# Optimization experiments

Hardware: AMD Instinct MI355X
Metric: run time of the kernel (lower is better)

## Reference

```python
import jax, jax.numpy as jnp
import numpy as np

N_HEADS = 32
WINDOW = 128  # each query t attends keys max(0, t-window) .. t inclusive (window+1 keys)


def _sliding_window_attention(x, Wq, Wk, Wv, Wo, n_heads=N_HEADS, window=WINDOW):
    B, T, D = x.shape
    H, dk = n_heads, D // n_heads
    bs = window            # block size = window -> each query block sees exactly 2 key blocks
    assert T % bs == 0
    nb = T // bs

    def heads(y):  # [B,T,D] -> [B,H,T,dk]
        return y.reshape(B, T, H, dk).transpose(0, 2, 1, 3)

    q = heads(x @ Wq.T)
    k = heads(x @ Wk.T)
    v = heads(x @ Wv.T)

    # Block queries: [B,H,nb,bs,dk]
    qb = q.reshape(B, H, nb, bs, dk)
    # Pad one zero block in front of keys/values, then build per-block 2-block windows.
    zpad = jnp.zeros((B, H, bs, dk), dtype=x.dtype)
    kp = jnp.concatenate([zpad, k], axis=2).reshape(B, H, nb + 1, bs, dk)
    vp = jnp.concatenate([zpad, v], axis=2).reshape(B, H, nb + 1, bs, dk)
    kw = jnp.concatenate([kp[:, :, :-1], kp[:, :, 1:]], axis=3)  # [B,H,nb,2bs,dk]
    vw = jnp.concatenate([vp[:, :, :-1], vp[:, :, 1:]], axis=3)

    scale = 1.0 / np.sqrt(dk).astype(np.float32)
    # scores: [B,H,nb,bs,2bs]
    scores = jnp.einsum('bhnrd,bhncd->bhnrc', qb, kw) * scale

    # Banded causal mask. Query global pos = i*bs + r, key global pos = (i-1)*bs + c.
    i = jnp.arange(nb)[:, None, None]
    r = jnp.arange(bs)[None, :, None]
    c = jnp.arange(2 * bs)[None, None, :]
    dist = (bs + r) - c                       # qpos - keypos
    key_global = i * bs - bs + c
    valid = (dist >= 0) & (dist <= window) & (key_global >= 0)  # [nb,bs,2bs]

    scores = jnp.where(valid[None, None], scores, jnp.finfo(scores.dtype).min)
    probs = jax.nn.softmax(scores, axis=-1)
    out = jnp.einsum('bhnrc,bhncd->bhnrd', probs, vw)           # [B,H,nb,bs,dk]
    out = out.reshape(B, H, T, dk).transpose(0, 2, 1, 3).reshape(B, T, D)
    return out @ Wo.T


def setup_inputs() -> dict:
    key = jax.random.key(0)
    ks = jax.random.split(key, 5)
    B, T, D = 2, 4096, 2048
    w_std = 0.02
    return {
        'x':  jax.random.normal(ks[0], (B, T, D), dtype=jnp.float32),
        'Wq': jax.random.normal(ks[1], (D, D), dtype=jnp.float32) * w_std,
        'Wk': jax.random.normal(ks[2], (D, D), dtype=jnp.float32) * w_std,
        'Wv': jax.random.normal(ks[3], (D, D), dtype=jnp.float32) * w_std,
        'Wo': jax.random.normal(ks[4], (D, D), dtype=jnp.float32) * w_std,
    }


def reference(x, Wq, Wk, Wv, Wo):
    return _sliding_window_attention(x, Wq, Wk, Wv, Wo)
```

## Files before the change

kernel.cpp:

```cpp
#include <hip/hip_runtime.h>
#include <hip/hip_bf16.h>

typedef __attribute__((ext_vector_type(8))) short bf16x8;
typedef __attribute__((ext_vector_type(8))) unsigned short ushort8;
typedef __attribute__((ext_vector_type(4))) float f32x4;
typedef __attribute__((ext_vector_type(2))) unsigned int u32x2;

#define MFMA16(a, b, c) __builtin_amdgcn_mfma_f32_16x16x32_bf16(a, b, c, 0, 0, 0)
#define CFENCE() asm volatile("" ::: "memory")

__device__ __forceinline__ unsigned short f2bf(float x) {
    unsigned u = __builtin_bit_cast(unsigned, x);
    u += 0x7FFFu + ((u >> 16) & 1u);
    return (unsigned short)(u >> 16);
}

__device__ __forceinline__ float fexp2(float x) {
#if __has_builtin(__builtin_amdgcn_exp2f)
    return __builtin_amdgcn_exp2f(x);
#else
    return exp2f(x);
#endif
}

__device__ __forceinline__ void gload16(const void* g, void* l) {
    __builtin_amdgcn_global_load_lds((const __attribute__((address_space(1))) void*)g,
                                     (__attribute__((address_space(3))) void*)l, 16, 0, 0);
}

__device__ __forceinline__ void bar() {
    asm volatile("" ::: "memory");
    __builtin_amdgcn_s_barrier();
    asm volatile("" ::: "memory");
}

#define WAITL() do { asm volatile("s_waitcnt lgkmcnt(0)" ::: "memory"); \
                     __builtin_amdgcn_sched_barrier(0); } while (0)

__global__ void cvt_f32_bf16(const float* __restrict__ src, unsigned short* __restrict__ dst, int n8) {
    int stride = gridDim.x * blockDim.x;
    for (int i = blockIdx.x * blockDim.x + threadIdx.x; i < n8; i += stride) {
        const float4* s = reinterpret_cast<const float4*>(src) + (size_t)i * 2;
        float4 a = s[0], b = s[1];
        ushort8 o;
        o[0] = f2bf(a.x); o[1] = f2bf(a.y); o[2] = f2bf(a.z); o[3] = f2bf(a.w);
        o[4] = f2bf(b.x); o[5] = f2bf(b.y); o[6] = f2bf(b.z); o[7] = f2bf(b.w);
        *(reinterpret_cast<ushort8*>(dst) + i) = o;
    }
}

#define QUAD(mg, ng, bfv)                                                         \
    do {                                                                          \
        _Pragma("unroll") for (int mm = 0; mm < 4; ++mm)                          \
        _Pragma("unroll") for (int nn = 0; nn < 2; ++nn)                          \
        _Pragma("unroll") for (int kk = 0; kk < 2; ++kk)                          \
            acc[(mg) * 4 + mm][(ng) * 2 + nn] =                                   \
                MFMA16(af[mm][kk], bfv[nn][kk], acc[(mg) * 4 + mm][(ng) * 2 + nn]); \
    } while (0)

template <int MODE>
__global__ __launch_bounds__(512, 2)
void gemm256(const unsigned short* __restrict__ A, const unsigned short* __restrict__ B,
             void* __restrict__ C, int M, int N, int K) {
    __shared__ char sm[131072];

    const int tid  = threadIdx.x;
    const int wid  = tid >> 6, lane = tid & 63;
    const int wr   = wid >> 2, wc = wid & 3;
    const int lrow = lane >> 4, lcol = lane & 15;

    const int flat = blockIdx.x;
    const int s = (flat & 7) * (gridDim.x >> 3) + (flat >> 3);
    const int nbn = N >> 8;
    const int bm = s / nbn, bn = s % nbn;

    const int srow = wid * 8 + (lane >> 3);
    const int scol = ((lane & 7) ^ ((lane >> 3) & 7)) * 8;
    const unsigned short* aS = A + (size_t)(bm * 256 + srow) * K + scol;
    const unsigned short* bS = B + (size_t)(bn * 256 + srow) * K + scol;
    const int ldsW = wid * 1024;

    auto stageA = [&](int d, int h, int t) {
#pragma unroll
        for (int q = 0; q < 2; ++q)
            gload16(aS + (size_t)(h * 128 + q * 64) * K + t * 64,
                    sm + d * 32768 + h * 16384 + ldsW + q * 8192);
    };
    auto stageB = [&](int d, int h, int t) {
#pragma unroll
        for (int q = 0; q < 2; ++q)
            gload16(bS + (size_t)(h * 128 + q * 64) * K + t * 64,
                    sm + 65536 + d * 32768 + h * 16384 + ldsW + q * 8192);
    };

    const int swz0 = (lrow * 16) ^ ((lcol & 7) << 4);
    const int swz1 = (64 + lrow * 16) ^ ((lcol & 7) << 4);
    const int ra = wr * 16 + lcol;
    const int rb = wc * 16 + lcol;

    bf16x8 af[4][2], bl[2][2], bh[2][2];
    auto loadA = [&](int d, int mg) {
#pragma unroll
        for (int mm = 0; mm < 4; ++mm) {
            af[mm][0] = *(const bf16x8*)(sm + d * 32768 + mg * 16384 + (mm * 32 + ra) * 128 + swz0);
            af[mm][1] = *(const bf16x8*)(sm + d * 32768 + mg * 16384 + (mm * 32 + ra) * 128 + swz1);
        }
    };
    auto loadB = [&](int d, int ng, bf16x8 (&bfv)[2][2]) {
#pragma unroll
        for (int nn = 0; nn < 2; ++nn) {
            bfv[nn][0] = *(const bf16x8*)(sm + 65536 + d * 32768 + ng * 16384 + (nn * 64 + rb) * 128 + swz0);
            bfv[nn][1] = *(const bf16x8*)(sm + 65536 + d * 32768 + ng * 16384 + (nn * 64 + rb) * 128 + swz1);
        }
    };

    f32x4 acc[8][4] = {};

    stageA(0, 0, 0); stageB(0, 0, 0); stageB(0, 1, 0); stageA(0, 1, 0);
    stageA(1, 0, 1); stageB(1, 0, 1); stageB(1, 1, 1);
    asm volatile("s_waitcnt vmcnt(6)" ::: "memory");
    bar();

    const int NI = K / 128;
#pragma unroll 1
    for (int i = 0; i < NI; ++i) {
        const int t0 = 2 * i;
        const bool last = (i == NI - 1);
        loadA(0, 0); loadB(0, 0, bl);
        stageA(1, 1, t0 + 1);
        bar(); WAITL();
        __builtin_amdgcn_s_setprio(1); QUAD(0, 0, bl); __builtin_amdgcn_s_setprio(0);
        bar();
        loadB(0, 1, bh);
        if (!last) stageA(0, 0, t0 + 2);
        bar(); WAITL();
        __builtin_amdgcn_s_setprio(1); QUAD(0, 1, bh); __builtin_amdgcn_s_setprio(0);
        bar();
        loadA(0, 1);
        if (!last) stageB(0, 0, t0 + 2);
        bar(); WAITL();
        __builtin_amdgcn_s_setprio(1); QUAD(1, 0, bl); __builtin_amdgcn_s_setprio(0);
        bar();
        if (!last) stageB(0, 1, t0 + 2);
        bar();
        __builtin_amdgcn_s_setprio(1); QUAD(1, 1, bh); __builtin_amdgcn_s_setprio(0);
        if (last) asm volatile("s_waitcnt vmcnt(0)" ::: "memory");
        else      asm volatile("s_waitcnt vmcnt(6)" ::: "memory");
        bar();
        loadA(1, 0); loadB(1, 0, bl);
        if (!last) stageA(0, 1, t0 + 2);
        bar(); WAITL();
        __builtin_amdgcn_s_setprio(1); QUAD(0, 0, bl); __builtin_amdgcn_s_setprio(0);
        bar();
        loadB(1, 1, bh);
        if (!last) stageA(1, 0, t0 + 3);
        bar(); WAITL();
        __builtin_amdgcn_s_setprio(1); QUAD(0, 1, bh); __builtin_amdgcn_s_setprio(0);
        bar();
        loadA(1, 1);
        if (!last) stageB(1, 0, t0 + 3);
        bar(); WAITL();
        __builtin_amdgcn_s_setprio(1); QUAD(1, 0, bl); __builtin_amdgcn_s_setprio(0);
        bar();
        if (!last) stageB(1, 1, t0 + 3);
        bar();
        __builtin_amdgcn_s_setprio(1); QUAD(1, 1, bh); __builtin_amdgcn_s_setprio(0);
        if (!last) asm volatile("s_waitcnt vmcnt(6)" ::: "memory");
        bar();
    }

    const size_t row0 = (size_t)bm * 256 + wr * 16 + lrow * 4;
    if (MODE == 1) {
        const int col0 = bn * 256 + wc * 16 + lcol;
#pragma unroll
        for (int m = 0; m < 8; ++m)
#pragma unroll
            for (int n = 0; n < 4; ++n)
#pragma unroll
                for (int r = 0; r < 4; ++r)
                    ((float*)C)[(row0 + m * 32 + r) * N + col0 + n * 64] = acc[m][n][r];
    } else {
        const int seg = (bn * 256) >> 11;
        const int coll = bn * 256 - seg * 2048 + wc * 16 + lcol;
        unsigned short* out = (unsigned short*)C + (size_t)seg * 16777216ull;
#pragma unroll
        for (int m = 0; m < 8; ++m)
#pragma unroll
            for (int n = 0; n < 4; ++n)
#pragma unroll
                for (int r = 0; r < 4; ++r)
                    out[(row0 + m * 32 + r) * 2048 + coll + n * 64] = f2bf(acc[m][n][r]);
    }
}

__global__ __launch_bounds__(256, 3)
void swa_attn(const unsigned short* __restrict__ Qb, const unsigned short* __restrict__ Kb,
              const unsigned short* __restrict__ Vb, unsigned short* __restrict__ Ob) {
    constexpr int T = 4096, D = 2048;
    constexpr float SC = 0.18033688011112042f;

    __shared__ unsigned short vt[64][136];
    __shared__ unsigned short pls[4][32][40];

    const int bid  = blockIdx.x;
    const int flat = (bid & 7) * 256 + (bid >> 3);
    const int i = flat & 31, h = (flat >> 5) & 31, b = flat >> 10;

    const int tid = threadIdx.x, wid = tid >> 6, lane = tid & 63;
    const int lcol = lane & 15, lrow = lane >> 4;

    const unsigned short* qp = Qb + (size_t)b * T * D + h * 64;
    const unsigned short* kp = Kb + (size_t)b * T * D + h * 64;
    const unsigned short* vp = Vb + (size_t)b * T * D + h * 64;

    const int t0 = (i == 0) ? 1 : 0;

    const int q0 = i * 128 + wid * 32;
    bf16x8 aq[2][2];
#pragma unroll
    for (int qg = 0; qg < 2; ++qg)
#pragma unroll
        for (int kf = 0; kf < 2; ++kf)
            aq[qg][kf] = *(const bf16x8*)(qp + (size_t)(q0 + qg * 16 + lcol) * D + kf * 32 + lrow * 8);

    f32x4 oacc[2][4] = {};
    float mrun[2] = {-1e30f, -1e30f}, lrun[2] = {0.f, 0.f};

#pragma unroll 1
    for (int t = t0; t < 2; ++t) {
        const int kt0 = (i - 1 + t) * 128;

#pragma unroll
        for (int it = 0; it < 4; ++it) {
            int e = it * 2048 + tid * 8;
            int kr = e >> 6;
            int dc = e & 63;
            bf16x8 v = *(const bf16x8*)(vp + (size_t)(kt0 + kr) * D + dc);
#pragma unroll
            for (int j = 0; j < 8; ++j) vt[dc + j][kr] = (unsigned short)v[j];
        }

        f32x4 s[2][8];
#pragma unroll
        for (int n = 0; n < 8; ++n) {
            const unsigned short* krow = kp + (size_t)(kt0 + n * 16 + lcol) * D + lrow * 8;
            bf16x8 k0 = *(const bf16x8*)(krow);
            bf16x8 k1 = *(const bf16x8*)(krow + 32);
            f32x4 z = {0.f, 0.f, 0.f, 0.f};
            s[0][n] = MFMA16(k1, aq[0][1], MFMA16(k0, aq[0][0], z));
            s[1][n] = MFMA16(k1, aq[1][1], MFMA16(k0, aq[1][0], z));
        }

#pragma unroll
        for (int qg = 0; qg < 2; ++qg) {
            const int q = wid * 32 + qg * 16 + lcol;
#pragma unroll
            for (int n = 0; n < 8; ++n) {
                const int cb = t * 128 + n * 16 + lrow * 4 - q;
#pragma unroll
                for (int r = 0; r < 4; ++r)
                    s[qg][n][r] = ((unsigned)(cb + r) <= 128u) ? s[qg][n][r] * SC : -1e30f;
            }
        }

#pragma unroll
        for (int qg = 0; qg < 2; ++qg) {
            float cm = -1e30f;
#pragma unroll
            for (int n = 0; n < 8; ++n)
#pragma unroll
                for (int r = 0; r < 4; ++r) cm = fmaxf(cm, s[qg][n][r]);
            cm = fmaxf(cm, __shfl_xor(cm, 16));
            cm = fmaxf(cm, __shfl_xor(cm, 32));
            const float mn = fmaxf(mrun[qg], cm);
            const float sf = fexp2(mrun[qg] - mn);
            mrun[qg] = mn;
            float rs = 0.f;
#pragma unroll
            for (int n = 0; n < 8; ++n)
#pragma unroll
                for (int r = 0; r < 4; ++r) {
                    float p = fexp2(s[qg][n][r] - mn);
                    s[qg][n][r] = p;
                    rs += p;
                }
            rs += __shfl_xor(rs, 16);
            rs += __shfl_xor(rs, 32);
            lrun[qg] = lrun[qg] * sf + rs;
#pragma unroll
            for (int nf = 0; nf < 4; ++nf) oacc[qg][nf] *= sf;
        }

        __syncthreads();

#pragma unroll
        for (int ks = 0; ks < 4; ++ks) {
            CFENCE();
#pragma unroll
            for (int qg = 0; qg < 2; ++qg) {
                unsigned short* prow = &pls[wid][qg * 16 + lcol][0];
#pragma unroll
                for (int r = 0; r < 4; ++r) {
                    prow[4 * lrow + r]      = f2bf(s[qg][2 * ks][r]);
                    prow[16 + 4 * lrow + r] = f2bf(s[qg][2 * ks + 1][r]);
                }
            }
            CFENCE();
            WAITL();
            bf16x8 pf0 = *(const bf16x8*)&pls[wid][lcol][lrow * 8];
            bf16x8 pf1 = *(const bf16x8*)&pls[wid][16 + lcol][lrow * 8];
#pragma unroll
            for (int nf = 0; nf < 4; ++nf) {
                bf16x8 av = *(const bf16x8*)&vt[nf * 16 + lcol][ks * 32 + lrow * 8];
                oacc[0][nf] = MFMA16(av, pf0, oacc[0][nf]);
                oacc[1][nf] = MFMA16(av, pf1, oacc[1][nf]);
            }
            CFENCE();
        }

        __syncthreads();
    }

#pragma unroll
    for (int qg = 0; qg < 2; ++qg) {
        const float inv = 1.f / lrun[qg];
        const int tok = i * 128 + wid * 32 + qg * 16 + lcol;
        unsigned short* orow = Ob + (size_t)(b * T + tok) * D + h * 64;
#pragma unroll
        for (int nf = 0; nf < 4; ++nf) {
            unsigned o0 = (unsigned)f2bf(oacc[qg][nf][0] * inv) |
                          ((unsigned)f2bf(oacc[qg][nf][1] * inv) << 16);
            unsigned o1 = (unsigned)f2bf(oacc[qg][nf][2] * inv) |
                          ((unsigned)f2bf(oacc[qg][nf][3] * inv) << 16);
            *(u32x2*)(orow + nf * 16 + lrow * 4) = (u32x2){o0, o1};
        }
    }
}

extern "C" void kernel_launch(void* const* d_in, const int* in_sizes, int n_in,
                              void* d_out, int out_size, void* d_ws, size_t ws_size,
                              hipStream_t stream) {
    const float* x  = (const float*)d_in[0];
    const float* Wq = (const float*)d_in[1];
    const float* Wk = (const float*)d_in[2];
    const float* Wv = (const float*)d_in[3];
    const float* Wo = (const float*)d_in[4];

    constexpr int B = 2, T = 4096, D = 2048;
    constexpr int M = B * T;
    constexpr size_t XE = (size_t)M * D;
    constexpr size_t WE = (size_t)D * D;

    char* ws = (char*)d_ws;
    unsigned short* xb  = (unsigned short*)(ws);
    unsigned short* wqb = (unsigned short*)(ws + XE * 2);
    unsigned short* wkb = (unsigned short*)(ws + XE * 2 + WE * 2);
    unsigned short* wvb = (unsigned short*)(ws + XE * 2 + WE * 4);
    unsigned short* wob = (unsigned short*)(ws + XE * 2 + WE * 6);
    unsigned short* qb  = (unsigned short*)(ws + XE * 2 + WE * 8);
    unsigned short* kb  = (unsigned short*)(ws + XE * 4 + WE * 8);
    unsigned short* vb  = (unsigned short*)(ws + XE * 6 + WE * 8);
    unsigned short* ab  = (unsigned short*)(ws + XE * 8 + WE * 8);

    cvt_f32_bf16<<<2048, 256, 0, stream>>>(x,  xb,  (int)(XE / 8));
    cvt_f32_bf16<<<2048, 256, 0, stream>>>(Wq, wqb, (int)(WE / 8));
    cvt_f32_bf16<<<2048, 256, 0, stream>>>(Wk, wkb, (int)(WE / 8));
    cvt_f32_bf16<<<2048, 256, 0, stream>>>(Wv, wvb, (int)(WE / 8));
    cvt_f32_bf16<<<2048, 256, 0, stream>>>(Wo, wob, (int)(WE / 8));

    gemm256<2><<<dim3((M / 256) * (6144 / 256)), 512, 0, stream>>>(xb, wqb, qb, M, 6144, D);

    swa_attn<<<dim3(2048), 256, 0, stream>>>(qb, kb, vb, ab);

    gemm256<1><<<dim3((M / 256) * (D / 256)), 512, 0, stream>>>(ab, wob, d_out, M, D, D);
}
```

Measured before the change: 358.3 us.

## Merge conversion launches, remap GEMM tiles per XCD, restage A prefetch

Replaces five separate fp32-to-bf16 conversion launches with one kernel covering x and all four weights in a contiguous workspace, which removes launch overhead and tail effects. Changes the GEMM block-to-tile mapping so each XCD owns a contiguous band of M rows and walks across N. This aims to improve L2 reuse of A tiles within an XCD. Moves the A-half prefetch (stageA(1,1)/(0,1)) into the same stage slot as the B prefetch and raises the vmcnt wait from 6 to 8, changing how global loads overlap with MFMA work.

```diff
diff --git a/kernel.cpp b/kernel.cpp
--- a/kernel.cpp
+++ b/kernel.cpp
@@ -37,10 +37,25 @@
 #define WAITL() do { asm volatile("s_waitcnt lgkmcnt(0)" ::: "memory"); \
                      __builtin_amdgcn_sched_barrier(0); } while (0)
 
-__global__ void cvt_f32_bf16(const float* __restrict__ src, unsigned short* __restrict__ dst, int n8) {
+__global__ void cvt_all(const float* __restrict__ x, const float* __restrict__ wq,
+                        const float* __restrict__ wk, const float* __restrict__ wv,
+                        const float* __restrict__ wo, unsigned short* __restrict__ dst,
+                        int total8) {
+    constexpr int XE8 = 2097152;
+    constexpr int WE8 = 524288;
     int stride = gridDim.x * blockDim.x;
-    for (int i = blockIdx.x * blockDim.x + threadIdx.x; i < n8; i += stride) {
-        const float4* s = reinterpret_cast<const float4*>(src) + (size_t)i * 2;
+    for (int i = blockIdx.x * blockDim.x + threadIdx.x; i < total8; i += stride) {
+        const float* src;
+        if (i < XE8) {
+            src = x + (size_t)i * 8;
+        } else {
+            int k = i - XE8;
+            int seg = k >> 19;
+            int off = k & (WE8 - 1);
+            const float* w = (seg == 0) ? wq : (seg == 1) ? wk : (seg == 2) ? wv : wo;
+            src = w + (size_t)off * 8;
+        }
+        const float4* s = (const float4*)src;
         float4 a = s[0], b = s[1];
         ushort8 o;
         o[0] = f2bf(a.x); o[1] = f2bf(a.y); o[2] = f2bf(a.z); o[3] = f2bf(a.w);
@@ -69,10 +84,12 @@
     const int wr   = wid >> 2, wc = wid & 3;
     const int lrow = lane >> 4, lcol = lane & 15;
 
-    const int flat = blockIdx.x;
-    const int s = (flat & 7) * (gridDim.x >> 3) + (flat >> 3);
-    const int nbn = N >> 8;
-    const int bm = s / nbn, bn = s % nbn;
+    const int nbm = M >> 8;
+    const int rpx = nbm >> 3;
+    const int xcd = blockIdx.x & 7;
+    const int l   = blockIdx.x >> 3;
+    const int bm  = xcd * rpx + (l & (rpx - 1));
+    const int bn  = l / rpx;
 
     const int srow = wid * 8 + (lane >> 3);
     const int scol = ((lane & 7) ^ ((lane >> 3) & 7)) * 8;
@@ -117,8 +134,8 @@
     f32x4 acc[8][4] = {};
 
     stageA(0, 0, 0); stageB(0, 0, 0); stageB(0, 1, 0); stageA(0, 1, 0);
-    stageA(1, 0, 1); stageB(1, 0, 1); stageB(1, 1, 1);
-    asm volatile("s_waitcnt vmcnt(6)" ::: "memory");
+    stageA(1, 0, 1); stageB(1, 0, 1); stageB(1, 1, 1); stageA(1, 1, 1);
+    asm volatile("s_waitcnt vmcnt(8)" ::: "memory");
     bar();
 
     const int NI = K / 128;
@@ -127,7 +144,6 @@
         const int t0 = 2 * i;
         const bool last = (i == NI - 1);
         loadA(0, 0); loadB(0, 0, bl);
-        stageA(1, 1, t0 + 1);
         bar(); WAITL();
         __builtin_amdgcn_s_setprio(1); QUAD(0, 0, bl); __builtin_amdgcn_s_setprio(0);
         bar();
@@ -141,14 +157,13 @@
         bar(); WAITL();
         __builtin_amdgcn_s_setprio(1); QUAD(1, 0, bl); __builtin_amdgcn_s_setprio(0);
         bar();
-        if (!last) stageB(0, 1, t0 + 2);
+        if (!last) { stageB(0, 1, t0 + 2); stageA(0, 1, t0 + 2); }
         bar();
         __builtin_amdgcn_s_setprio(1); QUAD(1, 1, bh); __builtin_amdgcn_s_setprio(0);
         if (last) asm volatile("s_waitcnt vmcnt(0)" ::: "memory");
-        else      asm volatile("s_waitcnt vmcnt(6)" ::: "memory");
+        else      asm volatile("s_waitcnt vmcnt(8)" ::: "memory");
         bar();
         loadA(1, 0); loadB(1, 0, bl);
-        if (!last) stageA(0, 1, t0 + 2);
         bar(); WAITL();
         __builtin_amdgcn_s_setprio(1); QUAD(0, 0, bl); __builtin_amdgcn_s_setprio(0);
         bar();
@@ -162,10 +177,10 @@
         bar(); WAITL();
         __builtin_amdgcn_s_setprio(1); QUAD(1, 0, bl); __builtin_amdgcn_s_setprio(0);
         bar();
-        if (!last) stageB(1, 1, t0 + 3);
+        if (!last) { stageB(1, 1, t0 + 3); stageA(1, 1, t0 + 3); }
         bar();
         __builtin_amdgcn_s_setprio(1); QUAD(1, 1, bh); __builtin_amdgcn_s_setprio(0);
-        if (!last) asm volatile("s_waitcnt vmcnt(6)" ::: "memory");
+        if (!last) asm volatile("s_waitcnt vmcnt(8)" ::: "memory");
         bar();
     }
 
@@ -354,23 +369,16 @@
     char* ws = (char*)d_ws;
     unsigned short* xb  = (unsigned short*)(ws);
     unsigned short* wqb = (unsigned short*)(ws + XE * 2);
-    unsigned short* wkb = (unsigned short*)(ws + XE * 2 + WE * 2);
-    unsigned short* wvb = (unsigned short*)(ws + XE * 2 + WE * 4);
-    unsigned short* wob = (unsigned short*)(ws + XE * 2 + WE * 6);
     unsigned short* qb  = (unsigned short*)(ws + XE * 2 + WE * 8);
     unsigned short* kb  = (unsigned short*)(ws + XE * 4 + WE * 8);
     unsigned short* vb  = (unsigned short*)(ws + XE * 6 + WE * 8);
     unsigned short* ab  = (unsigned short*)(ws + XE * 8 + WE * 8);
 
-    cvt_f32_bf16<<<2048, 256, 0, stream>>>(x,  xb,  (int)(XE / 8));
-    cvt_f32_bf16<<<2048, 256, 0, stream>>>(Wq, wqb, (int)(WE / 8));
-    cvt_f32_bf16<<<2048, 256, 0, stream>>>(Wk, wkb, (int)(WE / 8));
-    cvt_f32_bf16<<<2048, 256, 0, stream>>>(Wv, wvb, (int)(WE / 8));
-    cvt_f32_bf16<<<2048, 256, 0, stream>>>(Wo, wob, (int)(WE / 8));
+    cvt_all<<<2048, 256, 0, stream>>>(x, Wq, Wk, Wv, Wo, xb, (int)((XE + 4 * WE) / 8));
 
     gemm256<2><<<dim3((M / 256) * (6144 / 256)), 512, 0, stream>>>(xb, wqb, qb, M, 6144, D);
 
     swa_attn<<<dim3(2048), 256, 0, stream>>>(qb, kb, vb, ab);
 
-    gemm256<1><<<dim3((M / 256) * (D / 256)), 512, 0, stream>>>(ab, wob, d_out, M, D, D);
-}
+    gemm256<1><<<dim3((M / 256) * (D / 256)), 512, 0, stream>>>(ab, wqb + 3 * WE, d_out, M, D, D);
+}
```

After: 357.3 us. No clear change (-0.3%).
